# Kernel tuning notes

Measured on AMD Instinct MI355X. Metric: run time of the kernel, lower is better.

The kernel has to match this reference:

```python
import jax, jax.numpy as jnp
import numpy as np
import math

N_HEAD = 32
N_HEAD_KV = 8
HEAD_DIM = 64
ROTARY_DIM = 32  # partial rotary: applied to first ROTARY_DIM dims of each head
ROPE_BASE = 10000.0


def setup_inputs() -> dict:
    key = jax.random.key(0)
    ks = jax.random.split(key, 5)
    B, S, D = 1, 2048, N_HEAD * HEAD_DIM
    qkv_dim = (N_HEAD + 2 * N_HEAD_KV) * HEAD_DIM
    scale = 1.0 / math.sqrt(D)
    return {
        "x": jax.random.normal(ks[0], (B, S, D), dtype=jnp.float32),
        "Wqkv": jax.random.normal(ks[1], (D, qkv_dim), dtype=jnp.float32) * scale,
        "bqkv": jax.random.normal(ks[2], (qkv_dim,), dtype=jnp.float32) * 0.01,
        "Wout": jax.random.normal(ks[3], (D, D), dtype=jnp.float32) * scale,
        "bout": jax.random.normal(ks[4], (D,), dtype=jnp.float32) * 0.01,
    }


def _rope_cos_sin(seqlen):
    # inv_freq over half the rotary dims, positions in fp32 (pos_idx_in_fp32=True)
    inv_freq = 1.0 / (ROPE_BASE ** (jnp.arange(0, ROTARY_DIM, 2, dtype=jnp.float32) / ROTARY_DIM))
    t = jnp.arange(seqlen, dtype=jnp.float32)
    freqs = jnp.outer(t, inv_freq)  # [S, ROTARY_DIM//2]
    return jnp.cos(freqs), jnp.sin(freqs)


def _apply_rotary(x, cos, sin):
    # x: [B, S, H, head_dim]; rotate first ROTARY_DIM dims, pass the rest
    x_rot, x_pass = x[..., :ROTARY_DIM], x[..., ROTARY_DIM:]
    x1, x2 = jnp.split(x_rot, 2, axis=-1)
    c = cos[None, :, None, :]  # broadcast over batch and heads
    s = sin[None, :, None, :]
    x_rot = jnp.concatenate([x1 * c - x2 * s, x1 * s + x2 * c], axis=-1)
    return jnp.concatenate([x_rot.astype(x.dtype), x_pass], axis=-1)


def reference(x, Wqkv, bqkv, Wout, bout):
    B, S, D = x.shape
    # fused QKV projection
    qkv = x @ Wqkv + bqkv  # [B, S, (H + 2*Hkv) * hd]
    q = qkv[..., : N_HEAD * HEAD_DIM].reshape(B, S, N_HEAD, HEAD_DIM)
    kv = qkv[..., N_HEAD * HEAD_DIM :].reshape(B, S, 2, N_HEAD_KV, HEAD_DIM)

    cos, sin = _rope_cos_sin(S)
    q = _apply_rotary(q, cos, sin)
    k = _apply_rotary(kv[:, :, 0], cos, sin)  # rotary on K only (as in _apply_rotary_emb_kv)
    v = kv[:, :, 1]

    # GQA: repeat kv heads g times contiguously -> (hkv g)
    g = N_HEAD // N_HEAD_KV
    k = jnp.repeat(k, g, axis=2)  # [B, S, H, hd]
    v = jnp.repeat(v, g, axis=2)

    softmax_scale = 1.0 / math.sqrt(HEAD_DIM)
    scores = jnp.einsum("bthd,bshd->bhts", q.astype(jnp.float32), k.astype(jnp.float32) * softmax_scale)

    # causal mask with -10000 (matches torch masked_fill), seqlen_q == seqlen_k
    rows = jnp.arange(S)[:, None]
    cols = jnp.arange(S)[None, :]
    causal_mask = cols > rows  # [S, S]
    scores = jnp.where(causal_mask[None, None], jnp.float32(-10000.0), scores)

    attention = jax.nn.softmax(scores, axis=-1).astype(v.dtype)
    out = jnp.einsum("bhts,bshd->bthd", attention, v)  # [B, S, H, hd]
    out = out.reshape(B, S, N_HEAD * HEAD_DIM)
    return out @ Wout + bout
```

## Files before the change

### kernel.cpp

```cpp
#include <hip/hip_runtime.h>

typedef unsigned short ushort_t;
typedef __attribute__((ext_vector_type(8))) __bf16 bf16x8;
typedef __attribute__((ext_vector_type(4))) float f32x4;
typedef __attribute__((ext_vector_type(8))) unsigned short ushort8;
typedef __attribute__((ext_vector_type(4))) int int4v;

constexpr int S = 2048;
constexpr int D = 2048;
constexpr int NQKV = 3072;
constexpr int NH = 32, DH = 64;

static __device__ __forceinline__ float bf2f(ushort_t u) {
    return __uint_as_float(((unsigned int)u) << 16);
}
static __device__ __forceinline__ ushort_t f2bf(float f) {
    unsigned int u = __float_as_uint(f);
    u = (u + 0x7fffu + ((u >> 16) & 1u)) >> 16;
    return (ushort_t)u;
}

__global__ void k_cvt(const float* __restrict__ src, ushort_t* __restrict__ dst, int n4) {
    int i = blockIdx.x * blockDim.x + threadIdx.x;
    if (i < n4) {
        float4 v = ((const float4*)src)[i];
        ushort4 o;
        o.x = f2bf(v.x); o.y = f2bf(v.y); o.z = f2bf(v.z); o.w = f2bf(v.w);
        ((ushort4*)dst)[i] = o;
    }
}

__global__ void k_transpose_cvt(const float* __restrict__ src, ushort_t* __restrict__ dst,
                                int R, int C) {
    __shared__ float tile[32][33];
    int c0 = blockIdx.x * 32, r0 = blockIdx.y * 32;
    int tx = threadIdx.x, ty = threadIdx.y;
#pragma unroll
    for (int j = 0; j < 32; j += 8)
        tile[ty + j][tx] = src[(size_t)(r0 + ty + j) * C + c0 + tx];
    __syncthreads();
#pragma unroll
    for (int j = 0; j < 32; j += 8)
        dst[(size_t)(c0 + ty + j) * R + r0 + tx] = f2bf(tile[tx][ty + j]);
}

template <bool OUT_F32>
__global__ __launch_bounds__(256) void k_gemm(
    const ushort_t* __restrict__ A,
    const ushort_t* __restrict__ BT,
    const float* __restrict__ bias,
    void* __restrict__ Cout,
    int M, int N, int K)
{
    constexpr int BK = 32;
    __shared__ ushort_t As[128][BK + 8];
    __shared__ ushort_t Bs[128][BK + 8];
    const int m0 = blockIdx.y * 128;
    const int n0 = blockIdx.x * 128;
    const int t = threadIdx.x;
    const int lane = t & 63, wid = t >> 6;
    const int wm = (wid >> 1) * 64, wn = (wid & 1) * 64;
    const int lr = lane & 15, kg = (lane >> 4) * 8;

    f32x4 acc[4][4] = {};

    for (int k0 = 0; k0 < K; k0 += BK) {
#pragma unroll
        for (int i = 0; i < 2; ++i) {
            int id = t + i * 256;
            int r = id >> 2, kc = (id & 3) * 8;
            *(ushort8*)&As[r][kc] = *(const ushort8*)&A[(size_t)(m0 + r) * K + k0 + kc];
            *(ushort8*)&Bs[r][kc] = *(const ushort8*)&BT[(size_t)(n0 + r) * K + k0 + kc];
        }
        __syncthreads();
        bf16x8 af[4], bfr[4];
#pragma unroll
        for (int i = 0; i < 4; ++i) {
            af[i]  = *(const bf16x8*)&As[wm + i * 16 + lr][kg];
            bfr[i] = *(const bf16x8*)&Bs[wn + i * 16 + lr][kg];
        }
#pragma unroll
        for (int i = 0; i < 4; ++i)
#pragma unroll
            for (int j = 0; j < 4; ++j)
                acc[i][j] = __builtin_amdgcn_mfma_f32_16x16x32_bf16(af[i], bfr[j], acc[i][j], 0, 0, 0);
        __syncthreads();
    }

    const int lg = (lane >> 4) * 4;
#pragma unroll
    for (int j = 0; j < 4; ++j) {
        int n = n0 + wn + j * 16 + lr;
        float bv = bias[n];
#pragma unroll
        for (int i = 0; i < 4; ++i) {
#pragma unroll
            for (int r = 0; r < 4; ++r) {
                int m = m0 + wm + i * 16 + lg + r;
                float v = acc[i][j][r] + bv;
                if constexpr (OUT_F32) ((float*)Cout)[(size_t)m * N + n] = v;
                else ((ushort_t*)Cout)[(size_t)m * N + n] = f2bf(v);
            }
        }
    }
}

__global__ void k_rope(ushort_t* qkv) {
    int idx = blockIdx.x * blockDim.x + threadIdx.x;
    int i = idx & 15;
    int sh = idx >> 4;
    int h = sh % 40;
    int s = sh / 40;
    if (s >= S) return;
    int col = (h < 32) ? h * 64 : 2048 + (h - 32) * 64;
    ushort_t* p = qkv + (size_t)s * NQKV + col;
    float x1 = bf2f(p[i]), x2 = bf2f(p[i + 16]);
    float inv = exp2f(-(float)i * 0.83048202372f);
    float f = (float)s * inv;
    float c, sn;
    sincosf(f, &sn, &c);
    p[i]      = f2bf(x1 * c - x2 * sn);
    p[i + 16] = f2bf(x1 * sn + x2 * c);
}

__global__ __launch_bounds__(512) void k_attn(const ushort_t* __restrict__ qkv,
                                              ushort_t* __restrict__ out) {
    __shared__ ushort_t Ks[64 * 72];
    __shared__ ushort_t Vs[64 * 64];

    const int h = blockIdx.x;
    const int by = blockIdx.y;
    const int qb = (by & 1) ? (15 - (by >> 1)) : (by >> 1);
    const int q0 = qb * 128;
    const int kvh = h >> 2;
    const int t = threadIdx.x, lane = t & 63, w = t >> 6;
    const int lr = lane & 15, g = lane >> 4;
    const int qw = q0 + w * 16;
    const int qg = qw + lr;

    bf16x8 qf0, qf1;
    {
        const ushort_t* qp = qkv + (size_t)qg * NQKV + h * DH + g * 8;
        qf0 = *(const bf16x8*)&qp[0];
        qf1 = *(const bf16x8*)&qp[32];
    }
    const int idx0 = (lr + 16 * (2 * (g & 1))) << 2;
    const int idx1 = (lr + 16 * (2 * (g & 1) + 1)) << 2;
    const bool hi = (g >> 1) != 0;

    float mrun = -1e30f, lrun = 0.f;
    f32x4 o[4] = {};

    const int sr = t >> 3, sc = (t & 7) * 8;
    const ushort_t* gK = qkv + (size_t)sr * NQKV + 2048 + kvh * DH + sc;
    const ushort_t* gV = qkv + (size_t)sr * NQKV + 2560 + kvh * DH + sc;

    const int ntile = (q0 + 128) / 64;
    for (int kt = 0; kt < ntile; ++kt) {
        const int kv0 = kt * 64;
        {
            ushort8 kk = *(const ushort8*)&gK[(size_t)kv0 * NQKV];
            *(ushort8*)&Ks[sr * 72 + sc] = kk;
            ushort8 vv = *(const ushort8*)&gV[(size_t)kv0 * NQKV];
#pragma unroll
            for (int e = 0; e < 8; ++e) Vs[(sc + e) * 64 + (sr ^ sc)] = vv[e];
        }
        __syncthreads();
        if (kv0 <= qw) {
            f32x4 s[4];
#pragma unroll
            for (int nt = 0; nt < 4; ++nt) {
                bf16x8 a0 = *(const bf16x8*)&Ks[(nt * 16 + lr) * 72 + g * 8];
                bf16x8 a1 = *(const bf16x8*)&Ks[(nt * 16 + lr) * 72 + 32 + g * 8];
                f32x4 a = {};
                a = __builtin_amdgcn_mfma_f32_16x16x32_bf16(a0, qf0, a, 0, 0, 0);
                a = __builtin_amdgcn_mfma_f32_16x16x32_bf16(a1, qf1, a, 0, 0, 0);
                s[nt] = a;
            }
            float tmax = -3e38f;
#pragma unroll
            for (int nt = 0; nt < 4; ++nt)
#pragma unroll
                for (int r = 0; r < 4; ++r) {
                    float v = s[nt][r] * 0.125f;
                    int kvg = kv0 + nt * 16 + 4 * g + r;
                    v = (kvg > qg) ? -1e30f : v;
                    s[nt][r] = v;
                    tmax = fmaxf(tmax, v);
                }
            tmax = fmaxf(tmax, __shfl_xor(tmax, 16));
            tmax = fmaxf(tmax, __shfl_xor(tmax, 32));
            float mn = fmaxf(mrun, tmax);
            float alpha = __expf(mrun - mn);
            float sum = 0.f;
#pragma unroll
            for (int nt = 0; nt < 4; ++nt)
#pragma unroll
                for (int r = 0; r < 4; ++r) {
                    float p = __expf(s[nt][r] - mn);
                    s[nt][r] = p;
                    sum += p;
                }
            sum += __shfl_xor(sum, 16);
            sum += __shfl_xor(sum, 32);
            lrun = lrun * alpha + sum;
            mrun = mn;
#pragma unroll
            for (int tt = 0; tt < 4; ++tt) o[tt] *= alpha;

            int pk[8];
#pragma unroll
            for (int nt = 0; nt < 4; ++nt)
#pragma unroll
                for (int rp = 0; rp < 2; ++rp) {
                    int dd;
                    asm("v_cvt_pk_bf16_f32 %0, %1, %2"
                        : "=v"(dd) : "v"(s[nt][2 * rp]), "v"(s[nt][2 * rp + 1]));
                    pk[nt * 2 + rp] = dd;
                }
#pragma unroll
            for (int ks = 0; ks < 2; ++ks) {
                int a0 = __builtin_amdgcn_ds_bpermute(idx0, pk[(2 * ks) * 2 + 0]);
                int b0 = __builtin_amdgcn_ds_bpermute(idx0, pk[(2 * ks + 1) * 2 + 0]);
                int a1 = __builtin_amdgcn_ds_bpermute(idx0, pk[(2 * ks) * 2 + 1]);
                int b1 = __builtin_amdgcn_ds_bpermute(idx0, pk[(2 * ks + 1) * 2 + 1]);
                int a2 = __builtin_amdgcn_ds_bpermute(idx1, pk[(2 * ks) * 2 + 0]);
                int b2 = __builtin_amdgcn_ds_bpermute(idx1, pk[(2 * ks + 1) * 2 + 0]);
                int a3 = __builtin_amdgcn_ds_bpermute(idx1, pk[(2 * ks) * 2 + 1]);
                int b3 = __builtin_amdgcn_ds_bpermute(idx1, pk[(2 * ks + 1) * 2 + 1]);
                int4v pb;
                pb.x = hi ? b0 : a0;
                pb.y = hi ? b1 : a1;
                pb.z = hi ? b2 : a2;
                pb.w = hi ? b3 : a3;
                bf16x8 pf = __builtin_bit_cast(bf16x8, pb);
#pragma unroll
                for (int tt = 0; tt < 4; ++tt) {
                    const int dh = tt * 16 + lr;
                    bf16x8 va = *(const bf16x8*)&Vs[dh * 64 + ((32 * ks + g * 8) ^ (dh & 56))];
                    o[tt] = __builtin_amdgcn_mfma_f32_16x16x32_bf16(va, pf, o[tt], 0, 0, 0);
                }
            }
        }
        __syncthreads();
    }
    float inv = 1.0f / lrun;
    ushort_t* op = out + (size_t)qg * D + h * DH;
#pragma unroll
    for (int tt = 0; tt < 4; ++tt) {
#pragma unroll
        for (int rp = 0; rp < 2; ++rp) {
            int dd;
            float va = o[tt][2 * rp] * inv, vb = o[tt][2 * rp + 1] * inv;
            asm("v_cvt_pk_bf16_f32 %0, %1, %2" : "=v"(dd) : "v"(va), "v"(vb));
            *(int*)&op[tt * 16 + 4 * g + 2 * rp] = dd;
        }
    }
}

extern "C" void kernel_launch(void* const* d_in, const int* in_sizes, int n_in,
                              void* d_out, int out_size, void* d_ws, size_t ws_size,
                              hipStream_t stream) {
    const float* x    = (const float*)d_in[0];
    const float* Wqkv = (const float*)d_in[1];
    const float* bqkv = (const float*)d_in[2];
    const float* Wout = (const float*)d_in[3];
    const float* bout = (const float*)d_in[4];
    float* out = (float*)d_out;

    char* ws = (char*)d_ws;
    ushort_t* xb    = (ushort_t*)(ws);
    ushort_t* wqkvT = (ushort_t*)(ws + (8u  << 20));
    ushort_t* woutT = (ushort_t*)(ws + (20u << 20));
    ushort_t* qkvb  = (ushort_t*)(ws + (28u << 20));
    ushort_t* ao    = (ushort_t*)(ws + (40u << 20));

    k_cvt<<<(S * D / 4 + 255) / 256, 256, 0, stream>>>(x, xb, S * D / 4);
    k_transpose_cvt<<<dim3(NQKV / 32, D / 32), dim3(32, 8), 0, stream>>>(Wqkv, wqkvT, D, NQKV);
    k_transpose_cvt<<<dim3(D / 32, D / 32), dim3(32, 8), 0, stream>>>(Wout, woutT, D, D);
    k_gemm<false><<<dim3(NQKV / 128, S / 128), 256, 0, stream>>>(xb, wqkvT, bqkv, qkvb, S, NQKV, D);
    k_rope<<<(S * 40 * 16) / 256, 256, 0, stream>>>(qkvb);
    k_attn<<<dim3(NH, 16), 512, 0, stream>>>(qkvb, ao);
    k_gemm<true><<<dim3(D / 128, S / 128), 256, 0, stream>>>(ao, woutT, bout, out, S, D, D);
}
```

Baseline: 290.6 us.

## Load GEMM tiles directly into LDS and reorder attention query-block schedule

The GEMM tile loads now go straight from global memory into LDS through global_load_lds intrinsics, with 16 bytes per lane, instead of staging through registers and then storing to shared memory. The padded shared layout is dropped for a dense 32-wide row layout to match the direct-load addressing. That layout may add LDS bank conflicts on the fragment reads. Separately, the attention kernel's mapping from block index to query block changes from an interleaved heavy/light order to a different ordering.

New measurement: 283.0 us. -2.6%, faster.

```diff
diff --git a/kernel.cpp b/kernel.cpp
--- a/kernel.cpp
+++ b/kernel.cpp
@@ -19,6 +19,11 @@
     u = (u + 0x7fffu + ((u >> 16) & 1u)) >> 16;
     return (ushort_t)u;
 }
+
+#define GLD16(gp, sp)                                                          \
+    __builtin_amdgcn_global_load_lds(                                          \
+        (const __attribute__((address_space(1))) void*)(gp),                   \
+        (__attribute__((address_space(3))) void*)(sp), 16, 0, 0)
 
 __global__ void k_cvt(const float* __restrict__ src, ushort_t* __restrict__ dst, int n4) {
     int i = blockIdx.x * blockDim.x + threadIdx.x;
@@ -53,8 +58,8 @@
     int M, int N, int K)
 {
     constexpr int BK = 32;
-    __shared__ ushort_t As[128][BK + 8];
-    __shared__ ushort_t Bs[128][BK + 8];
+    __shared__ ushort_t As[128 * BK];
+    __shared__ ushort_t Bs[128 * BK];
     const int m0 = blockIdx.y * 128;
     const int n0 = blockIdx.x * 128;
     const int t = threadIdx.x;
@@ -62,22 +67,26 @@
     const int wm = (wid >> 1) * 64, wn = (wid & 1) * 64;
     const int lr = lane & 15, kg = (lane >> 4) * 8;
 
+    const int srow = lane >> 2;
+    const int scol = (lane & 3) * 8;
+    const ushort_t* gA = A + (size_t)(m0 + wid * 32 + srow) * K + scol;
+    const ushort_t* gB = BT + (size_t)(n0 + wid * 32 + srow) * K + scol;
+    ushort_t* lA = &As[(wid * 32) * BK];
+    ushort_t* lB = &Bs[(wid * 32) * BK];
+
     f32x4 acc[4][4] = {};
 
     for (int k0 = 0; k0 < K; k0 += BK) {
-#pragma unroll
-        for (int i = 0; i < 2; ++i) {
-            int id = t + i * 256;
-            int r = id >> 2, kc = (id & 3) * 8;
-            *(ushort8*)&As[r][kc] = *(const ushort8*)&A[(size_t)(m0 + r) * K + k0 + kc];
-            *(ushort8*)&Bs[r][kc] = *(const ushort8*)&BT[(size_t)(n0 + r) * K + k0 + kc];
-        }
+        GLD16(gA + k0, lA);
+        GLD16(gA + (size_t)16 * K + k0, lA + 16 * BK);
+        GLD16(gB + k0, lB);
+        GLD16(gB + (size_t)16 * K + k0, lB + 16 * BK);
         __syncthreads();
         bf16x8 af[4], bfr[4];
 #pragma unroll
         for (int i = 0; i < 4; ++i) {
-            af[i]  = *(const bf16x8*)&As[wm + i * 16 + lr][kg];
-            bfr[i] = *(const bf16x8*)&Bs[wn + i * 16 + lr][kg];
+            af[i]  = *(const bf16x8*)&As[(wm + i * 16 + lr) * BK + kg];
+            bfr[i] = *(const bf16x8*)&Bs[(wn + i * 16 + lr) * BK + kg];
         }
 #pragma unroll
         for (int i = 0; i < 4; ++i)
@@ -130,7 +139,7 @@
 
     const int h = blockIdx.x;
     const int by = blockIdx.y;
-    const int qb = (by & 1) ? (15 - (by >> 1)) : (by >> 1);
+    const int qb = (by < 8) ? by : 23 - by;
     const int q0 = qb * 128;
     const int kvh = h >> 2;
     const int t = threadIdx.x, lane = t & 63, w = t >> 6;
```
